# Performance work log

Hardware: AMD Instinct MI355X
Metric: run time of the kernel (lower is better)

The kernel has to match this reference:

```python
import jax, jax.numpy as jnp
import numpy as np

WIN = 11      # window_size
SIGMA = 1.5
CH = 1        # channel
LEVELS = 5
C1 = 0.01 ** 2
C2 = 0.03 ** 2
MS_WEIGHTS = np.array([0.0448, 0.2856, 0.3001, 0.2363, 0.1333], dtype=np.float32)


def _gaussian_window(dtype):
    x = jnp.arange(WIN, dtype=jnp.float32) - WIN // 2
    g = jnp.exp(-(x ** 2) / (2.0 * SIGMA ** 2))
    g = g / g.sum()
    w2 = jnp.outer(g, g)  # [K, K]
    # depthwise kernel [C, 1, K, K]
    return jnp.broadcast_to(w2[None, None], (CH, 1, WIN, WIN)).astype(dtype)


def _blur(x, w):
    # depthwise 11x11 Gaussian blur, SAME padding (= pad window_size//2)
    return jax.lax.conv_general_dilated(
        x, w, window_strides=(1, 1), padding='SAME',
        dimension_numbers=('NCHW', 'OIHW', 'NCHW'),
        feature_group_count=CH)


def _ssim_level(img1, img2, w):
    mu1 = _blur(img1, w)
    mu2 = _blur(img2, w)
    mu1_sq = mu1 * mu1
    mu2_sq = mu2 * mu2
    mu1_mu2 = mu1 * mu2
    sigma1_sq = _blur(img1 * img1, w) - mu1_sq
    sigma2_sq = _blur(img2 * img2, w) - mu2_sq
    sigma12 = _blur(img1 * img2, w) - mu1_mu2
    denom_c = sigma1_sq + sigma2_sq + C2
    mcs_map = (2.0 * sigma12 + C2) / denom_c
    ssim_map = ((2.0 * mu1_mu2 + C1) / (mu1_sq + mu2_sq + C1)) * mcs_map
    return ssim_map.mean(), mcs_map.mean()


def _avg_pool2(x):
    B, C, H, W = x.shape
    return x.reshape(B, C, H // 2, 2, W // 2, 2).mean(axis=(3, 5))


def reference(img1, img2):
    w = _gaussian_window(img1.dtype)
    weights = jnp.asarray(MS_WEIGHTS, dtype=img1.dtype)
    mssim, mcs = [], []
    for _ in range(LEVELS):  # small fixed loop over pyramid levels
        s, m = _ssim_level(img1, img2, w)
        mssim.append(s)
        mcs.append(m)
        img1 = _avg_pool2(img1)
        img2 = _avg_pool2(img2)
    mssim = jnp.stack(mssim)
    mcs = jnp.stack(mcs)
    return jnp.prod(mcs[:LEVELS - 1] ** weights[:LEVELS - 1]) * mssim[LEVELS - 1] ** weights[LEVELS - 1]


def setup_inputs() -> dict:
    key = jax.random.key(0)
    k1, k2 = jax.random.split(key)
    img1 = jax.random.uniform(k1, (32, 1, 512, 512), dtype=jnp.float32)
    # correlated second image so ssim/mcs means stay positive (fractional powers)
    img2 = jnp.clip(img1 + 0.1 * jax.random.normal(k2, img1.shape, dtype=jnp.float32), 0.0, 1.0)
    return {"img1": img1, "img2": img2}
```

## Files before the change

kernel.cpp:

```cpp
#include <hip/hip_runtime.h>
#include <math.h>


typedef float v2f __attribute__((ext_vector_type(2)));

#define TILE 32
#define HALO 5
#define SROWS 42
#define SMEM_FLOATS 6728

struct GaussW { float w[11]; };

#define C1_ (0.01f * 0.01f)
#define C2_ (0.03f * 0.03f)

__device__ __forceinline__ void ssim_tile(
        const float* __restrict__ p1, const float* __restrict__ p2,
        int W, int W0, bool poolL0,
        int tile_x, int tile_y, const GaussW& gw,
        float2* __restrict__ resslot, float* smem, int tid) {
    v2f* hb01 = (v2f*)smem;
    v2f* hb23 = (v2f*)(smem + 2 * SROWS * TILE);
    float* hb4 = smem + 4 * SROWS * TILE;
    float* red = smem + 5 * SROWS * TILE;

    const bool xfast = (tile_x >= 8) && (tile_x + TILE + 8 <= W);

    for (int it = tid; it < SROWS * 8; it += 256) {
        int r = it >> 3, c4 = it & 7;
        int gy = tile_y + r - HALO;
        int gx0 = tile_x + (c4 << 2) - 8;
        bool rowok = (gy >= 0) && (gy < W);
        float a1[20], a2[20];
#pragma unroll
        for (int i = 0; i < 20; i++) { a1[i] = 0.f; a2[i] = 0.f; }
        if (!poolL0) {
            const float* row1 = p1 + (size_t)gy * W;
            const float* row2 = p2 + (size_t)gy * W;
            if (xfast) {
                if (rowok) {
#pragma unroll
                    for (int q = 0; q < 5; q++) {
                        float4 v1 = *(const float4*)(row1 + gx0 + q * 4);
                        float4 v2v = *(const float4*)(row2 + gx0 + q * 4);
                        a1[q*4+0] = v1.x;  a1[q*4+1] = v1.y;  a1[q*4+2] = v1.z;  a1[q*4+3] = v1.w;
                        a2[q*4+0] = v2v.x; a2[q*4+1] = v2v.y; a2[q*4+2] = v2v.z; a2[q*4+3] = v2v.w;
                    }
                }
            } else {
#pragma unroll
                for (int q = 0; q < 5; q++) {
                    int g = gx0 + q * 4;
                    if (rowok && g >= 0 && g + 4 <= W) {
                        float4 v1 = *(const float4*)(row1 + g);
                        float4 v2v = *(const float4*)(row2 + g);
                        a1[q*4+0] = v1.x;  a1[q*4+1] = v1.y;  a1[q*4+2] = v1.z;  a1[q*4+3] = v1.w;
                        a2[q*4+0] = v2v.x; a2[q*4+1] = v2v.y; a2[q*4+2] = v2v.z; a2[q*4+3] = v2v.w;
                    }
                }
            }
        } else {
            const float* r10 = p1 + (size_t)(2 * gy) * W0;
            const float* r11 = r10 + W0;
            const float* r20 = p2 + (size_t)(2 * gy) * W0;
            const float* r21 = r20 + W0;
#pragma unroll
            for (int q = 0; q < 5; q++) {
                int g = gx0 + q * 4;
                bool ok = rowok && (xfast || (g >= 0 && g + 4 <= W));
                if (ok) {
                    float4 f0 = *(const float4*)(r10 + 2 * g);
                    float4 f1 = *(const float4*)(r10 + 2 * g + 4);
                    float4 f2 = *(const float4*)(r11 + 2 * g);
                    float4 f3 = *(const float4*)(r11 + 2 * g + 4);
                    a1[q*4+0] = 0.25f * (f0.x + f0.y + f2.x + f2.y);
                    a1[q*4+1] = 0.25f * (f0.z + f0.w + f2.z + f2.w);
                    a1[q*4+2] = 0.25f * (f1.x + f1.y + f3.x + f3.y);
                    a1[q*4+3] = 0.25f * (f1.z + f1.w + f3.z + f3.w);
                    float4 g0 = *(const float4*)(r20 + 2 * g);
                    float4 g1 = *(const float4*)(r20 + 2 * g + 4);
                    float4 g2 = *(const float4*)(r21 + 2 * g);
                    float4 g3 = *(const float4*)(r21 + 2 * g + 4);
                    a2[q*4+0] = 0.25f * (g0.x + g0.y + g2.x + g2.y);
                    a2[q*4+1] = 0.25f * (g0.z + g0.w + g2.z + g2.w);
                    a2[q*4+2] = 0.25f * (g1.x + g1.y + g3.x + g3.y);
                    a2[q*4+3] = 0.25f * (g1.z + g1.w + g3.z + g3.w);
                }
            }
        }
        v2f A[20];
#pragma unroll
        for (int i = 0; i < 20; i++) A[i] = (v2f){a1[i], a2[i]};
        v2f P[14];
        float p12[14];
#pragma unroll
        for (int i = 0; i < 14; i++) {
            v2f u = A[i + 3];
            P[i] = u * u;
            p12[i] = u.x * u.y;
        }
        v2f h01[4] = {(v2f)(0.f), (v2f)(0.f), (v2f)(0.f), (v2f)(0.f)};
        v2f h23[4] = {(v2f)(0.f), (v2f)(0.f), (v2f)(0.f), (v2f)(0.f)};
        float h4[4] = {0.f, 0.f, 0.f, 0.f};
#pragma unroll
        for (int k = 0; k < 11; k++) {
            float wk = gw.w[k];
#pragma unroll
            for (int j = 0; j < 4; j++) {
                h01[j] += wk * A[3 + j + k];
                h23[j] += wk * P[j + k];
                h4[j]  += wk * p12[j + k];
            }
        }
        int ob = r * TILE + (c4 << 2);
#pragma unroll
        for (int j = 0; j < 4; j++) { hb01[ob + j] = h01[j]; hb23[ob + j] = h23[j]; }
        *(float4*)&hb4[ob] = make_float4(h4[0], h4[1], h4[2], h4[3]);
    }
    __syncthreads();

    float ssim_v = 0.f, mcs_v = 0.f;
    {
        int tx = tid & 31, y0 = (tid >> 5) * 4;
        v2f m01[4], m23[4];
        float m4[4];
        {
            v2f v[14];
#pragma unroll
            for (int r = 0; r < 14; r++) v[r] = hb01[(y0 + r) * TILE + tx];
#pragma unroll
            for (int j = 0; j < 4; j++) {
                v2f s = (v2f)(0.f);
#pragma unroll
                for (int k = 0; k < 11; k++) s += gw.w[k] * v[j + k];
                m01[j] = s;
            }
        }
        {
            v2f v[14];
#pragma unroll
            for (int r = 0; r < 14; r++) v[r] = hb23[(y0 + r) * TILE + tx];
#pragma unroll
            for (int j = 0; j < 4; j++) {
                v2f s = (v2f)(0.f);
#pragma unroll
                for (int k = 0; k < 11; k++) s += gw.w[k] * v[j + k];
                m23[j] = s;
            }
        }
        {
            float v[14];
#pragma unroll
            for (int r = 0; r < 14; r++) v[r] = hb4[(y0 + r) * TILE + tx];
#pragma unroll
            for (int j = 0; j < 4; j++) {
                float s = 0.f;
#pragma unroll
                for (int k = 0; k < 11; k++) s += gw.w[k] * v[j + k];
                m4[j] = s;
            }
        }
#pragma unroll
        for (int j = 0; j < 4; j++) {
            float mu1 = m01[j].x, mu2 = m01[j].y;
            float mu1sq = mu1 * mu1, mu2sq = mu2 * mu2, mu12 = mu1 * mu2;
            float sg11 = m23[j].x - mu1sq;
            float sg22 = m23[j].y - mu2sq;
            float sg12 = m4[j] - mu12;
            float mcs  = (2.f * sg12 + C2_) / (sg11 + sg22 + C2_);
            float ssim = ((2.f * mu12 + C1_) / (mu1sq + mu2sq + C1_)) * mcs;
            ssim_v += ssim;
            mcs_v  += mcs;
        }
    }

#pragma unroll
    for (int off = 32; off > 0; off >>= 1) {
        ssim_v += __shfl_down(ssim_v, off);
        mcs_v  += __shfl_down(mcs_v, off);
    }
    int wave = tid >> 6, lane = tid & 63;
    if (lane == 0) { red[wave] = ssim_v; red[4 + wave] = mcs_v; }
    __syncthreads();
    if (tid == 0) {
        float S = red[0] + red[1] + red[2] + red[3];
        float M = red[4] + red[5] + red[6] + red[7];
        *resslot = make_float2(S, M);
    }
}

__device__ __forceinline__ void pyramid_region(
        const float* __restrict__ in1, const float* __restrict__ in2,
        int n, int reg,
        float* __restrict__ l2a, float* __restrict__ l2b,
        float* __restrict__ l3a, float* __restrict__ l3b,
        float* __restrict__ l4a, float* __restrict__ l4b,
        float* smem, int tid) {
    float* b1 = smem;
    float* b2 = smem + 1024;
    float* c1 = smem + 2048;
    float* c2 = smem + 2304;
    float* d1 = smem + 2560;
    float* d2 = smem + 2624;
    const int rx = reg & 7, ry = reg >> 3;
    const float* p1 = in1 + (size_t)n * 512 * 512;
    const float* p2 = in2 + (size_t)n * 512 * 512;

    for (int i = tid; i < 32 * 16; i += 256) {
        int oy = i >> 4, oxp = i & 15;
        int gy = ry * 64 + 2 * oy, gx = rx * 64 + 4 * oxp;
        float4 r10 = *(const float4*)(p1 + (size_t)gy * 512 + gx);
        float4 r11 = *(const float4*)(p1 + (size_t)(gy + 1) * 512 + gx);
        float4 r20 = *(const float4*)(p2 + (size_t)gy * 512 + gx);
        float4 r21 = *(const float4*)(p2 + (size_t)(gy + 1) * 512 + gx);
        *(float2*)&b1[oy * 32 + 2 * oxp] =
            make_float2(0.25f * (r10.x + r10.y + r11.x + r11.y),
                        0.25f * (r10.z + r10.w + r11.z + r11.w));
        *(float2*)&b2[oy * 32 + 2 * oxp] =
            make_float2(0.25f * (r20.x + r20.y + r21.x + r21.y),
                        0.25f * (r20.z + r20.w + r21.z + r21.w));
    }
    __syncthreads();
    if (tid < 16 * 8) {
        int oy = tid >> 3, oxp = tid & 7;
        float4 r10 = *(const float4*)&b1[(2 * oy) * 32 + 4 * oxp];
        float4 r11 = *(const float4*)&b1[(2 * oy + 1) * 32 + 4 * oxp];
        float4 r20 = *(const float4*)&b2[(2 * oy) * 32 + 4 * oxp];
        float4 r21 = *(const float4*)&b2[(2 * oy + 1) * 32 + 4 * oxp];
        float2 o1 = make_float2(0.25f * (r10.x + r10.y + r11.x + r11.y),
                                0.25f * (r10.z + r10.w + r11.z + r11.w));
        float2 o2 = make_float2(0.25f * (r20.x + r20.y + r21.x + r21.y),
                                0.25f * (r20.z + r20.w + r21.z + r21.w));
        *(float2*)&c1[oy * 16 + 2 * oxp] = o1;
        *(float2*)&c2[oy * 16 + 2 * oxp] = o2;
        size_t o = (size_t)n * 128 * 128 + (size_t)(ry * 16 + oy) * 128 + rx * 16 + 2 * oxp;
        *(float2*)&l2a[o] = o1;
        *(float2*)&l2b[o] = o2;
    }
    __syncthreads();
    if (tid < 8 * 4) {
        int oy = tid >> 2, oxp = tid & 3;
        float4 r10 = *(const float4*)&c1[(2 * oy) * 16 + 4 * oxp];
        float4 r11 = *(const float4*)&c1[(2 * oy + 1) * 16 + 4 * oxp];
        float4 r20 = *(const float4*)&c2[(2 * oy) * 16 + 4 * oxp];
        float4 r21 = *(const float4*)&c2[(2 * oy + 1) * 16 + 4 * oxp];
        float2 o1 = make_float2(0.25f * (r10.x + r10.y + r11.x + r11.y),
                                0.25f * (r10.z + r10.w + r11.z + r11.w));
        float2 o2 = make_float2(0.25f * (r20.x + r20.y + r21.x + r21.y),
                                0.25f * (r20.z + r20.w + r21.z + r21.w));
        *(float2*)&d1[oy * 8 + 2 * oxp] = o1;
        *(float2*)&d2[oy * 8 + 2 * oxp] = o2;
        size_t o = (size_t)n * 64 * 64 + (size_t)(ry * 8 + oy) * 64 + rx * 8 + 2 * oxp;
        *(float2*)&l3a[o] = o1;
        *(float2*)&l3b[o] = o2;
    }
    __syncthreads();
    if (tid < 4 * 2) {
        int oy = tid >> 1, oxp = tid & 1;
        float4 r10 = *(const float4*)&d1[(2 * oy) * 8 + 4 * oxp];
        float4 r11 = *(const float4*)&d1[(2 * oy + 1) * 8 + 4 * oxp];
        float4 r20 = *(const float4*)&d2[(2 * oy) * 8 + 4 * oxp];
        float4 r21 = *(const float4*)&d2[(2 * oy + 1) * 8 + 4 * oxp];
        float2 o1 = make_float2(0.25f * (r10.x + r10.y + r11.x + r11.y),
                                0.25f * (r10.z + r10.w + r11.z + r11.w));
        float2 o2 = make_float2(0.25f * (r20.x + r20.y + r21.x + r21.y),
                                0.25f * (r20.z + r20.w + r21.z + r21.w));
        size_t o = (size_t)n * 32 * 32 + (size_t)(ry * 4 + oy) * 32 + rx * 4 + 2 * oxp;
        *(float2*)&l4a[o] = o1;
        *(float2*)&l4b[o] = o2;
    }
}

__global__ __launch_bounds__(256, 4) void d1_kernel(
        const float* __restrict__ i0a, const float* __restrict__ i0b,
        float* __restrict__ l2a, float* __restrict__ l2b,
        float* __restrict__ l3a, float* __restrict__ l3b,
        float* __restrict__ l4a, float* __restrict__ l4b,
        float2* __restrict__ res0, float2* __restrict__ res1, GaussW gw) {
    __shared__ float smem[SMEM_FLOATS];
    const int tid = threadIdx.x;
    const int t = blockIdx.x;
    const int n = blockIdx.y;
    const float* p1 = i0a + (size_t)n * 512 * 512;
    const float* p2 = i0b + (size_t)n * 512 * 512;
    if (t < 64) {
        pyramid_region(i0a, i0b, n, t, l2a, l2b, l3a, l3b, l4a, l4b, smem, tid);
    } else if (t < 320) {
        int idx = t - 64;
        ssim_tile(p1, p2, 512, 512, false, (idx & 15) << 5, (idx >> 4) << 5,
                  gw, &res0[n * 256 + idx], smem, tid);
    } else {
        int idx = t - 320;
        ssim_tile(p1, p2, 256, 512, true, (idx & 7) << 5, (idx >> 3) << 5,
                  gw, &res1[n * 64 + idx], smem, tid);
    }
}

__global__ __launch_bounds__(256, 4) void d2_kernel(
        const float* __restrict__ l2a, const float* __restrict__ l2b,
        const float* __restrict__ l3a, const float* __restrict__ l3b,
        const float* __restrict__ l4a, const float* __restrict__ l4b,
        float2* __restrict__ res2, float2* __restrict__ res3,
        float2* __restrict__ res4, GaussW gw) {
    __shared__ float smem[SMEM_FLOATS];
    const int tid = threadIdx.x;
    const int t = blockIdx.x;
    const int n = blockIdx.y;
    const float* b1;
    const float* b2;
    int W, tx, ty;
    float2* slot;
    if (t < 16)      { W = 128; b1 = l2a; b2 = l2b; tx = (t & 3) << 5; ty = (t >> 2) << 5; slot = &res2[n * 16 + t]; }
    else if (t < 20) { int i = t - 16; W = 64; b1 = l3a; b2 = l3b; tx = (i & 1) << 5; ty = (i >> 1) << 5; slot = &res3[n * 4 + i]; }
    else             { W = 32; b1 = l4a; b2 = l4b; tx = 0; ty = 0; slot = &res4[n]; }
    ssim_tile(b1 + (size_t)n * W * W, b2 + (size_t)n * W * W, W, W, false,
              tx, ty, gw, slot, smem, tid);
}

__global__ void finalize_kernel(const float2* __restrict__ res0,
                                const float2* __restrict__ res1,
                                const float2* __restrict__ res2,
                                const float2* __restrict__ res3,
                                const float2* __restrict__ res4,
                                float* __restrict__ out, int N) {
    __shared__ float2 redf[5][4];
    const int tid = threadIdx.x;
    const float2* rr[5] = {res0, res1, res2, res3, res4};
    const int cnts[5] = {N * 256, N * 64, N * 16, N * 4, N};
#pragma unroll
    for (int l = 0; l < 5; l++) {
        float sx = 0.f, sy = 0.f;
        for (int i = tid; i < cnts[l]; i += 256) {
            float2 v = rr[l][i];
            sx += v.x;
            sy += v.y;
        }
#pragma unroll
        for (int off = 32; off > 0; off >>= 1) {
            sx += __shfl_down(sx, off);
            sy += __shfl_down(sy, off);
        }
        if ((tid & 63) == 0) redf[l][tid >> 6] = make_float2(sx, sy);
    }
    __syncthreads();
    if (tid == 0) {
        const float wts[5] = {0.0448f, 0.2856f, 0.3001f, 0.2363f, 0.1333f};
        float r = 1.f;
#pragma unroll
        for (int l = 0; l < 5; l++) {
            float sx = redf[l][0].x + redf[l][1].x + redf[l][2].x + redf[l][3].x;
            float sy = redf[l][0].y + redf[l][1].y + redf[l][2].y + redf[l][3].y;
            int Hl = 512 >> l;
            float cnt = (float)N * (float)Hl * (float)Hl;
            float ssim_m = sx / cnt;
            float mcs_m  = sy / cnt;
            if (l < 4) r *= powf(mcs_m, wts[l]);
            else       r *= powf(ssim_m, wts[4]);
        }
        out[0] = r;
    }
}

extern "C" void kernel_launch(void* const* d_in, const int* in_sizes, int n_in,
                              void* d_out, int out_size, void* d_ws, size_t ws_size,
                              hipStream_t stream) {
    const float* img1 = (const float*)d_in[0];
    const float* img2 = (const float*)d_in[1];
    float* out = (float*)d_out;
    const int HW0 = 512 * 512;
    const int N = in_sizes[0] / HW0;

    float* base = (float*)d_ws;
    size_t cur = 0;
    float* l2a = base + cur; cur += (size_t)N * 128 * 128;
    float* l2b = base + cur; cur += (size_t)N * 128 * 128;
    float* l3a = base + cur; cur += (size_t)N * 64 * 64;
    float* l3b = base + cur; cur += (size_t)N * 64 * 64;
    float* l4a = base + cur; cur += (size_t)N * 32 * 32;
    float* l4b = base + cur; cur += (size_t)N * 32 * 32;
    float2* res0 = (float2*)(base + cur); cur += (size_t)N * 512;
    float2* res1 = (float2*)(base + cur); cur += (size_t)N * 128;
    float2* res2 = (float2*)(base + cur); cur += (size_t)N * 32;
    float2* res3 = (float2*)(base + cur); cur += (size_t)N * 8;
    float2* res4 = (float2*)(base + cur); cur += (size_t)N * 2;

    GaussW gw;
    {
        double g[11], sum = 0.0;
        for (int i = 0; i < 11; i++) {
            double x = (double)(i - 5);
            g[i] = exp(-(x * x) / (2.0 * 1.5 * 1.5));
            sum += g[i];
        }
        for (int i = 0; i < 11; i++) gw.w[i] = (float)(g[i] / sum);
    }

    d1_kernel<<<dim3(384, N), 256, 0, stream>>>(
        img1, img2, l2a, l2b, l3a, l3b, l4a, l4b, res0, res1, gw);
    d2_kernel<<<dim3(21, N), 256, 0, stream>>>(
        l2a, l2b, l3a, l3b, l4a, l4b, res2, res3, res4, gw);
    finalize_kernel<<<1, 256, 0, stream>>>(res0, res1, res2, res3, res4, out, N);
}
```

Measured before the change: 186.0 us.

## Materialize level-1 pyramid, move its SSIM to second kernel, fuse finalize

The level-0 pass now writes the 2x-pooled level-1 images to workspace, so level-1 SSIM tiles read them directly instead of re-pooling from full-resolution inputs inside the first kernel. Level-1 tiles move into the second kernel alongside levels 2-4. The separate finalize launch is replaced by a last-block-done atomic counter in the second kernel. Launch bounds go from 4 to 6 blocks per CU. This drops redundant 4x input reads and a kernel launch, at the cost of extra workspace traffic for level 1, a serialized final reduction in one block, and possible register pressure from the higher occupancy target.

Result: slower. 233.1 us (+25.3%).

```diff
diff --git a/kernel.cpp b/kernel.cpp
--- a/kernel.cpp
+++ b/kernel.cpp
@@ -16,8 +16,7 @@
 
 __device__ __forceinline__ void ssim_tile(
         const float* __restrict__ p1, const float* __restrict__ p2,
-        int W, int W0, bool poolL0,
-        int tile_x, int tile_y, const GaussW& gw,
+        int W, int tile_x, int tile_y, const GaussW& gw,
         float2* __restrict__ resslot, float* smem, int tid) {
     v2f* hb01 = (v2f*)smem;
     v2f* hb23 = (v2f*)(smem + 2 * SROWS * TILE);
@@ -31,60 +30,30 @@
         int gy = tile_y + r - HALO;
         int gx0 = tile_x + (c4 << 2) - 8;
         bool rowok = (gy >= 0) && (gy < W);
+        const float* row1 = p1 + (size_t)gy * W;
+        const float* row2 = p2 + (size_t)gy * W;
         float a1[20], a2[20];
 #pragma unroll
         for (int i = 0; i < 20; i++) { a1[i] = 0.f; a2[i] = 0.f; }
-        if (!poolL0) {
-            const float* row1 = p1 + (size_t)gy * W;
-            const float* row2 = p2 + (size_t)gy * W;
-            if (xfast) {
-                if (rowok) {
-#pragma unroll
-                    for (int q = 0; q < 5; q++) {
-                        float4 v1 = *(const float4*)(row1 + gx0 + q * 4);
-                        float4 v2v = *(const float4*)(row2 + gx0 + q * 4);
-                        a1[q*4+0] = v1.x;  a1[q*4+1] = v1.y;  a1[q*4+2] = v1.z;  a1[q*4+3] = v1.w;
-                        a2[q*4+0] = v2v.x; a2[q*4+1] = v2v.y; a2[q*4+2] = v2v.z; a2[q*4+3] = v2v.w;
-                    }
+        if (xfast) {
+            if (rowok) {
+#pragma unroll
+                for (int q = 0; q < 5; q++) {
+                    float4 v1 = *(const float4*)(row1 + gx0 + q * 4);
+                    float4 v2v = *(const float4*)(row2 + gx0 + q * 4);
+                    a1[q*4+0] = v1.x;  a1[q*4+1] = v1.y;  a1[q*4+2] = v1.z;  a1[q*4+3] = v1.w;
+                    a2[q*4+0] = v2v.x; a2[q*4+1] = v2v.y; a2[q*4+2] = v2v.z; a2[q*4+3] = v2v.w;
                 }
-            } else {
-#pragma unroll
-                for (int q = 0; q < 5; q++) {
-                    int g = gx0 + q * 4;
-                    if (rowok && g >= 0 && g + 4 <= W) {
-                        float4 v1 = *(const float4*)(row1 + g);
-                        float4 v2v = *(const float4*)(row2 + g);
-                        a1[q*4+0] = v1.x;  a1[q*4+1] = v1.y;  a1[q*4+2] = v1.z;  a1[q*4+3] = v1.w;
-                        a2[q*4+0] = v2v.x; a2[q*4+1] = v2v.y; a2[q*4+2] = v2v.z; a2[q*4+3] = v2v.w;
-                    }
-                }
             }
         } else {
-            const float* r10 = p1 + (size_t)(2 * gy) * W0;
-            const float* r11 = r10 + W0;
-            const float* r20 = p2 + (size_t)(2 * gy) * W0;
-            const float* r21 = r20 + W0;
 #pragma unroll
             for (int q = 0; q < 5; q++) {
                 int g = gx0 + q * 4;
-                bool ok = rowok && (xfast || (g >= 0 && g + 4 <= W));
-                if (ok) {
-                    float4 f0 = *(const float4*)(r10 + 2 * g);
-                    float4 f1 = *(const float4*)(r10 + 2 * g + 4);
-                    float4 f2 = *(const float4*)(r11 + 2 * g);
-                    float4 f3 = *(const float4*)(r11 + 2 * g + 4);
-                    a1[q*4+0] = 0.25f * (f0.x + f0.y + f2.x + f2.y);
-                    a1[q*4+1] = 0.25f * (f0.z + f0.w + f2.z + f2.w);
-                    a1[q*4+2] = 0.25f * (f1.x + f1.y + f3.x + f3.y);
-                    a1[q*4+3] = 0.25f * (f1.z + f1.w + f3.z + f3.w);
-                    float4 g0 = *(const float4*)(r20 + 2 * g);
-                    float4 g1 = *(const float4*)(r20 + 2 * g + 4);
-                    float4 g2 = *(const float4*)(r21 + 2 * g);
-                    float4 g3 = *(const float4*)(r21 + 2 * g + 4);
-                    a2[q*4+0] = 0.25f * (g0.x + g0.y + g2.x + g2.y);
-                    a2[q*4+1] = 0.25f * (g0.z + g0.w + g2.z + g2.w);
-                    a2[q*4+2] = 0.25f * (g1.x + g1.y + g3.x + g3.y);
-                    a2[q*4+3] = 0.25f * (g1.z + g1.w + g3.z + g3.w);
+                if (rowok && g >= 0 && g + 4 <= W) {
+                    float4 v1 = *(const float4*)(row1 + g);
+                    float4 v2v = *(const float4*)(row2 + g);
+                    a1[q*4+0] = v1.x;  a1[q*4+1] = v1.y;  a1[q*4+2] = v1.z;  a1[q*4+3] = v1.w;
+                    a2[q*4+0] = v2v.x; a2[q*4+1] = v2v.y; a2[q*4+2] = v2v.z; a2[q*4+3] = v2v.w;
                 }
             }
         }
@@ -192,6 +161,7 @@
 __device__ __forceinline__ void pyramid_region(
         const float* __restrict__ in1, const float* __restrict__ in2,
         int n, int reg,
+        float* __restrict__ l1a, float* __restrict__ l1b,
         float* __restrict__ l2a, float* __restrict__ l2b,
         float* __restrict__ l3a, float* __restrict__ l3b,
         float* __restrict__ l4a, float* __restrict__ l4b,
@@ -213,12 +183,15 @@
         float4 r11 = *(const float4*)(p1 + (size_t)(gy + 1) * 512 + gx);
         float4 r20 = *(const float4*)(p2 + (size_t)gy * 512 + gx);
         float4 r21 = *(const float4*)(p2 + (size_t)(gy + 1) * 512 + gx);
-        *(float2*)&b1[oy * 32 + 2 * oxp] =
-            make_float2(0.25f * (r10.x + r10.y + r11.x + r11.y),
-                        0.25f * (r10.z + r10.w + r11.z + r11.w));
-        *(float2*)&b2[oy * 32 + 2 * oxp] =
-            make_float2(0.25f * (r20.x + r20.y + r21.x + r21.y),
-                        0.25f * (r20.z + r20.w + r21.z + r21.w));
+        float2 o1 = make_float2(0.25f * (r10.x + r10.y + r11.x + r11.y),
+                                0.25f * (r10.z + r10.w + r11.z + r11.w));
+        float2 o2 = make_float2(0.25f * (r20.x + r20.y + r21.x + r21.y),
+                                0.25f * (r20.z + r20.w + r21.z + r21.w));
+        *(float2*)&b1[oy * 32 + 2 * oxp] = o1;
+        *(float2*)&b2[oy * 32 + 2 * oxp] = o2;
+        size_t o = (size_t)n * 256 * 256 + (size_t)(ry * 32 + oy) * 256 + rx * 32 + 2 * oxp;
+        *(float2*)&l1a[o] = o1;
+        *(float2*)&l1b[o] = o2;
     }
     __syncthreads();
     if (tid < 16 * 8) {
@@ -271,38 +244,43 @@
     }
 }
 
-__global__ __launch_bounds__(256, 4) void d1_kernel(
+__global__ __launch_bounds__(256, 6) void d1_kernel(
         const float* __restrict__ i0a, const float* __restrict__ i0b,
+        float* __restrict__ l1a, float* __restrict__ l1b,
         float* __restrict__ l2a, float* __restrict__ l2b,
         float* __restrict__ l3a, float* __restrict__ l3b,
         float* __restrict__ l4a, float* __restrict__ l4b,
-        float2* __restrict__ res0, float2* __restrict__ res1, GaussW gw) {
+        float2* __restrict__ res0, unsigned* __restrict__ ctr, GaussW gw) {
     __shared__ float smem[SMEM_FLOATS];
     const int tid = threadIdx.x;
     const int t = blockIdx.x;
     const int n = blockIdx.y;
-    const float* p1 = i0a + (size_t)n * 512 * 512;
-    const float* p2 = i0b + (size_t)n * 512 * 512;
+    if (t == 0 && n == 0 && tid == 0) *ctr = 0;
     if (t < 64) {
-        pyramid_region(i0a, i0b, n, t, l2a, l2b, l3a, l3b, l4a, l4b, smem, tid);
-    } else if (t < 320) {
+        pyramid_region(i0a, i0b, n, t, l1a, l1b, l2a, l2b, l3a, l3b, l4a, l4b,
+                       smem, tid);
+    } else {
         int idx = t - 64;
-        ssim_tile(p1, p2, 512, 512, false, (idx & 15) << 5, (idx >> 4) << 5,
+        const float* p1 = i0a + (size_t)n * 512 * 512;
+        const float* p2 = i0b + (size_t)n * 512 * 512;
+        ssim_tile(p1, p2, 512, (idx & 15) << 5, (idx >> 4) << 5,
                   gw, &res0[n * 256 + idx], smem, tid);
-    } else {
-        int idx = t - 320;
-        ssim_tile(p1, p2, 256, 512, true, (idx & 7) << 5, (idx >> 3) << 5,
-                  gw, &res1[n * 64 + idx], smem, tid);
-    }
-}
-
-__global__ __launch_bounds__(256, 4) void d2_kernel(
+    }
+}
+
+#define D2_GRIDX 85
+
+__global__ __launch_bounds__(256, 6) void d2_kernel(
+        const float* __restrict__ l1a, const float* __restrict__ l1b,
         const float* __restrict__ l2a, const float* __restrict__ l2b,
         const float* __restrict__ l3a, const float* __restrict__ l3b,
         const float* __restrict__ l4a, const float* __restrict__ l4b,
+        float2* __restrict__ res0, float2* __restrict__ res1,
         float2* __restrict__ res2, float2* __restrict__ res3,
-        float2* __restrict__ res4, GaussW gw) {
+        float2* __restrict__ res4, unsigned* __restrict__ ctr,
+        float* __restrict__ out, int N, GaussW gw) {
     __shared__ float smem[SMEM_FLOATS];
+    __shared__ int islast;
     const int tid = threadIdx.x;
     const int t = blockIdx.x;
     const int n = blockIdx.y;
@@ -310,54 +288,56 @@
     const float* b2;
     int W, tx, ty;
     float2* slot;
-    if (t < 16)      { W = 128; b1 = l2a; b2 = l2b; tx = (t & 3) << 5; ty = (t >> 2) << 5; slot = &res2[n * 16 + t]; }
-    else if (t < 20) { int i = t - 16; W = 64; b1 = l3a; b2 = l3b; tx = (i & 1) << 5; ty = (i >> 1) << 5; slot = &res3[n * 4 + i]; }
+    if (t < 64)      { W = 256; b1 = l1a; b2 = l1b; tx = (t & 7) << 5; ty = (t >> 3) << 5; slot = &res1[n * 64 + t]; }
+    else if (t < 80) { int i = t - 64; W = 128; b1 = l2a; b2 = l2b; tx = (i & 3) << 5; ty = (i >> 2) << 5; slot = &res2[n * 16 + i]; }
+    else if (t < 84) { int i = t - 80; W = 64; b1 = l3a; b2 = l3b; tx = (i & 1) << 5; ty = (i >> 1) << 5; slot = &res3[n * 4 + i]; }
     else             { W = 32; b1 = l4a; b2 = l4b; tx = 0; ty = 0; slot = &res4[n]; }
-    ssim_tile(b1 + (size_t)n * W * W, b2 + (size_t)n * W * W, W, W, false,
+    ssim_tile(b1 + (size_t)n * W * W, b2 + (size_t)n * W * W, W,
               tx, ty, gw, slot, smem, tid);
-}
-
-__global__ void finalize_kernel(const float2* __restrict__ res0,
-                                const float2* __restrict__ res1,
-                                const float2* __restrict__ res2,
-                                const float2* __restrict__ res3,
-                                const float2* __restrict__ res4,
-                                float* __restrict__ out, int N) {
-    __shared__ float2 redf[5][4];
-    const int tid = threadIdx.x;
-    const float2* rr[5] = {res0, res1, res2, res3, res4};
-    const int cnts[5] = {N * 256, N * 64, N * 16, N * 4, N};
-#pragma unroll
-    for (int l = 0; l < 5; l++) {
-        float sx = 0.f, sy = 0.f;
-        for (int i = tid; i < cnts[l]; i += 256) {
-            float2 v = rr[l][i];
-            sx += v.x;
-            sy += v.y;
-        }
-#pragma unroll
-        for (int off = 32; off > 0; off >>= 1) {
-            sx += __shfl_down(sx, off);
-            sy += __shfl_down(sy, off);
-        }
-        if ((tid & 63) == 0) redf[l][tid >> 6] = make_float2(sx, sy);
-    }
-    __syncthreads();
+
     if (tid == 0) {
-        const float wts[5] = {0.0448f, 0.2856f, 0.3001f, 0.2363f, 0.1333f};
-        float r = 1.f;
+        __threadfence();
+        unsigned old = atomicAdd(ctr, 1u);
+        islast = (old == (unsigned)(D2_GRIDX * N - 1)) ? 1 : 0;
+    }
+    __syncthreads();
+    if (islast) {
+        __threadfence();
+        __shared__ float2 redf[5][4];
+        const float2* rr[5] = {res0, res1, res2, res3, res4};
+        const int cnts[5] = {N * 256, N * 64, N * 16, N * 4, N};
 #pragma unroll
         for (int l = 0; l < 5; l++) {
-            float sx = redf[l][0].x + redf[l][1].x + redf[l][2].x + redf[l][3].x;
-            float sy = redf[l][0].y + redf[l][1].y + redf[l][2].y + redf[l][3].y;
-            int Hl = 512 >> l;
-            float cnt = (float)N * (float)Hl * (float)Hl;
-            float ssim_m = sx / cnt;
-            float mcs_m  = sy / cnt;
-            if (l < 4) r *= powf(mcs_m, wts[l]);
-            else       r *= powf(ssim_m, wts[4]);
-        }
-        out[0] = r;
+            float sx = 0.f, sy = 0.f;
+            for (int i = tid; i < cnts[l]; i += 256) {
+                float2 v = rr[l][i];
+                sx += v.x;
+                sy += v.y;
+            }
+#pragma unroll
+            for (int off = 32; off > 0; off >>= 1) {
+                sx += __shfl_down(sx, off);
+                sy += __shfl_down(sy, off);
+            }
+            if ((tid & 63) == 0) redf[l][tid >> 6] = make_float2(sx, sy);
+        }
+        __syncthreads();
+        if (tid == 0) {
+            const float wts[5] = {0.0448f, 0.2856f, 0.3001f, 0.2363f, 0.1333f};
+            float r = 1.f;
+#pragma unroll
+            for (int l = 0; l < 5; l++) {
+                float sx = redf[l][0].x + redf[l][1].x + redf[l][2].x + redf[l][3].x;
+                float sy = redf[l][0].y + redf[l][1].y + redf[l][2].y + redf[l][3].y;
+                int Hl = 512 >> l;
+                float cnt = (float)N * (float)Hl * (float)Hl;
+                float ssim_m = sx / cnt;
+                float mcs_m  = sy / cnt;
+                if (l < 4) r *= powf(mcs_m, wts[l]);
+                else       r *= powf(ssim_m, wts[4]);
+            }
+            out[0] = r;
+        }
     }
 }
 
@@ -372,6 +352,8 @@
 
     float* base = (float*)d_ws;
     size_t cur = 0;
+    float* l1a = base + cur; cur += (size_t)N * 256 * 256;
+    float* l1b = base + cur; cur += (size_t)N * 256 * 256;
     float* l2a = base + cur; cur += (size_t)N * 128 * 128;
     float* l2b = base + cur; cur += (size_t)N * 128 * 128;
     float* l3a = base + cur; cur += (size_t)N * 64 * 64;
@@ -383,6 +365,7 @@
     float2* res2 = (float2*)(base + cur); cur += (size_t)N * 32;
     float2* res3 = (float2*)(base + cur); cur += (size_t)N * 8;
     float2* res4 = (float2*)(base + cur); cur += (size_t)N * 2;
+    unsigned* ctr = (unsigned*)(base + cur); cur += 2;
 
     GaussW gw;
     {
@@ -395,9 +378,9 @@
         for (int i = 0; i < 11; i++) gw.w[i] = (float)(g[i] / sum);
     }
 
-    d1_kernel<<<dim3(384, N), 256, 0, stream>>>(
-        img1, img2, l2a, l2b, l3a, l3b, l4a, l4b, res0, res1, gw);
-    d2_kernel<<<dim3(21, N), 256, 0, stream>>>(
-        l2a, l2b, l3a, l3b, l4a, l4b, res2, res3, res4, gw);
-    finalize_kernel<<<1, 256, 0, stream>>>(res0, res1, res2, res3, res4, out, N);
-}
+    d1_kernel<<<dim3(320, N), 256, 0, stream>>>(
+        img1, img2, l1a, l1b, l2a, l2b, l3a, l3b, l4a, l4b, res0, ctr, gw);
+    d2_kernel<<<dim3(D2_GRIDX, N), 256, 0, stream>>>(
+        l1a, l1b, l2a, l2b, l3a, l3b, l4a, l4b,
+        res0, res1, res2, res3, res4, ctr, out, N, gw);
+}
```
